# Kernel optimization log

Hardware: AMD Instinct MI355X
Metric: run time of the kernel (lower is better)

Reference implementation:

```python
import jax, jax.numpy as jnp
import numpy as np
from jax import lax

EPS = 1e-9
DN = ('NCHW', 'OIHW', 'NCHW')


def _conv2d_valid(x, w):
    return lax.conv_general_dilated(x, w, window_strides=(1, 1), padding='VALID',
                                    dimension_numbers=DN)


def setup_inputs() -> dict:
    key = jax.random.key(0)
    kx, ky = jax.random.split(key)
    x = jax.random.normal(kx, (32, 64, 96, 96), dtype=jnp.float32)
    y = jax.random.normal(ky, (32, 64, 13, 13), dtype=jnp.float32)  # (K prototypes, C, kh, kw)
    return {'x': x, 'y': y}


def reference(x, y):
    # Per-prototype L2 normalization of y over (C, kh, kw)
    y_norm = jnp.clip(jnp.sqrt(jnp.sum(y * y, axis=(1, 2, 3), keepdims=True)), EPS)
    normed_y = y / y_norm
    # Sliding-window L2 norm of x. The torch code convolves x^2 with ones of
    # shape (K, C, kh, kw) producing K identical channels; we compute one
    # channel and broadcast (same math, less work).
    ones_k = jnp.ones((1,) + y.shape[1:], dtype=x.dtype)
    x_norm = jnp.clip(jnp.sqrt(_conv2d_valid(x * x, ones_k)), EPS)  # (B,1,H',W')
    diss = _conv2d_valid(x, normed_y) / x_norm  # (B,K,H',W')
    return jax.nn.relu(diss)
```

## Files before the change

### kernel.cpp

```cpp
#include <hip/hip_runtime.h>
#include <hip/hip_bf16.h>

#define B_   32
#define C_   64
#define H_   96
#define W_   96
#define K_   32
#define R_   13
#define HO_  84
#define WO_  84
#define HW_  (H_*W_)
#define OHW_ (HO_*WO_)
#define CRR_ (C_*R_*R_)
#define RR_  (R_*R_)

#define TILE_ 16
#define PW_   28
#define NPIX_ (PW_*PW_)
#define RPAD_ 13312
#define BUF_  (2*RPAD_)
#define LDS_NEW (2*BUF_)
#define REGB_ (NPIX_*16)
#define LDS_FB (2*REGB_)

#define XBF_BYTES  ((size_t)B_*4*HW_*32)
#define UG_BYTES   ((size_t)RR_*4096)
#define S_BYTES    ((size_t)B_*HW_*4)
#define INV_BYTES  ((size_t)B_*OHW_*4)
#define WS_NEED    (XBF_BYTES + UG_BYTES + S_BYTES + INV_BYTES)

typedef unsigned int u32;
typedef unsigned short u16;
typedef __attribute__((ext_vector_type(16))) float f32x16;
typedef __attribute__((ext_vector_type(4))) u32 u32x4;

static __device__ __forceinline__ u16 f2bf(float v){
    __hip_bfloat16 h = __float2bfloat16(v);
    return *reinterpret_cast<u16*>(&h);
}

#define MFMA(acc, a, b) asm("v_mfma_f32_32x32x16_bf16 %0, %1, %2, %0" \
                            : "+v"(acc) : "v"(a), "v"(b))

static __device__ __forceinline__ void gload_lds16(const void* g, void* l){
    __builtin_amdgcn_global_load_lds(
        (const __attribute__((address_space(1))) unsigned char*)g,
        (__attribute__((address_space(3))) unsigned char*)l, 16, 0, 0);
}

__global__ void k_prep_y(const float* __restrict__ y, unsigned char* __restrict__ u_g){
    int k = blockIdx.x, tid = threadIdx.x;
    const float* yk = y + (size_t)k * CRR_;
    float ss = 0.f;
    for (int idx = tid; idx < CRR_; idx += 256){ float v = yk[idx]; ss += v*v; }
    for (int off = 32; off; off >>= 1) ss += __shfl_down(ss, off);
    __shared__ float red[4];
    if ((tid & 63) == 0) red[tid >> 6] = ss;
    __syncthreads();
    float inv = 1.f / fmaxf(sqrtf(red[0]+red[1]+red[2]+red[3]), 1e-9f);

    int c = tid & 63, grp = tid >> 6;
    int inoff = (k << 5) | ((c & 15) << 1);
    for (int base = 0; base < RR_; base += 4){
        int ij = base + grp;
        if (ij < RR_){
            int i = ij / R_, jx = ij % R_;
            float v = yk[c*RR_ + ij] * inv;
            size_t slice = ((size_t)(c >> 4) * RR_ + jx*R_ + i) << 10;
            *(u16*)(u_g + slice + inoff) = f2bf(v);
        }
    }
}

__global__ void k_sqcvt(const float* __restrict__ x, float* __restrict__ s,
                        unsigned char* __restrict__ xbf){
    int idx = blockIdx.x*256 + threadIdx.x;
    int b = idx / HW_, r = idx % HW_;
    const float* xb = x + (size_t)b * C_ * HW_ + r;
    float acc = 0.f;
    #pragma unroll
    for (int q = 0; q < 4; ++q){
        int c0 = q*16;
        float a0 = xb[(size_t)(c0+0)*HW_],  a1 = xb[(size_t)(c0+1)*HW_];
        float a2 = xb[(size_t)(c0+2)*HW_],  a3 = xb[(size_t)(c0+3)*HW_];
        float a4 = xb[(size_t)(c0+4)*HW_],  a5 = xb[(size_t)(c0+5)*HW_];
        float a6 = xb[(size_t)(c0+6)*HW_],  a7 = xb[(size_t)(c0+7)*HW_];
        float a8 = xb[(size_t)(c0+8)*HW_],  a9 = xb[(size_t)(c0+9)*HW_];
        float aa = xb[(size_t)(c0+10)*HW_], ab = xb[(size_t)(c0+11)*HW_];
        float ac = xb[(size_t)(c0+12)*HW_], ad = xb[(size_t)(c0+13)*HW_];
        float ae = xb[(size_t)(c0+14)*HW_], af = xb[(size_t)(c0+15)*HW_];
        acc += a0*a0+a1*a1+a2*a2+a3*a3+a4*a4+a5*a5+a6*a6+a7*a7
             + a8*a8+a9*a9+aa*aa+ab*ab+ac*ac+ad*ad+ae*ae+af*af;
        u32x4 q0 = { f2bf(a0)|((u32)f2bf(a1)<<16), f2bf(a2)|((u32)f2bf(a3)<<16),
                     f2bf(a4)|((u32)f2bf(a5)<<16), f2bf(a6)|((u32)f2bf(a7)<<16) };
        u32x4 q1 = { f2bf(a8)|((u32)f2bf(a9)<<16), f2bf(aa)|((u32)f2bf(ab)<<16),
                     f2bf(ac)|((u32)f2bf(ad)<<16), f2bf(ae)|((u32)f2bf(af)<<16) };
        unsigned char* ob = xbf + ((size_t)(b*4 + q)*HW_ + r)*32;
        *(u32x4*)(ob)      = q0;
        *(u32x4*)(ob + 16) = q1;
    }
    s[idx] = acc;
}

__global__ void k_sq(const float* __restrict__ x, float* __restrict__ s){
    int idx = blockIdx.x*256 + threadIdx.x;
    int b = idx / HW_, r = idx % HW_;
    const float* xb = x + (size_t)b * C_ * HW_;
    float acc = 0.f;
    #pragma unroll
    for (int c = 0; c < C_; ++c){ float v = xb[(size_t)c*HW_ + r]; acc += v*v; }
    s[idx] = acc;
}

__global__ void k_inv(const float* __restrict__ s, float* __restrict__ inv_xn){
    int idx = blockIdx.x*256 + threadIdx.x;
    int b = idx / OHW_, r = idx % OHW_;
    int oh = r / WO_, ow = r % WO_;
    const float* sb = s + (size_t)b*HW_ + oh*W_ + ow;
    float acc = 0.f;
    for (int i = 0; i < R_; ++i){
        #pragma unroll
        for (int j = 0; j < R_; ++j) acc += sb[i*W_ + j];
    }
    inv_xn[idx] = 1.f / fmaxf(sqrtf(acc), 1e-9f);
}

__launch_bounds__(256, 4)
__global__ void k_main(const unsigned char* __restrict__ xbf,
                       const unsigned char* __restrict__ u_g,
                       const float* __restrict__ inv_xn, float* __restrict__ out){
    extern __shared__ unsigned char lds[];

    int bb0 = blockIdx.x;
    int bb  = (bb0 & 7) * 144 + (bb0 >> 3);
    int b  = bb / 36;
    int tt = bb % 36;
    int oy = (tt / 6) * TILE_;
    int ox = (tt % 6) * TILE_;

    int tid  = threadIdx.x;
    int lane = tid & 63;
    int wv   = tid >> 6;
    int ks   = lane >> 5;
    int rb   = (lane >> 4) & 1;
    int cx   = lane & 15;
    int kpr  = lane & 31;

    const unsigned char* xq = xbf + (size_t)b*4*HW_*32;
    int aoff = (kpr << 5) + (ks << 4);
    int pb   = (4*wv + rb) * PW_ + cx;

    int goff[13];
    #pragma unroll
    for (int cb = 0; cb < 13; ++cb){
        int p = cb*64 + lane; if (p > NPIX_-1) p = NPIX_-1;
        int py = p / PW_, px = p % PW_;
        int gy = oy + py; if (gy > H_-1) gy = H_-1;
        int gx = ox + px; if (gx > W_-1) gx = W_-1;
        goff[cb] = (gy*W_ + gx) << 5;
    }

#define STAGE(bufsel, q) {                                                   \
        const unsigned char* src = xq + (size_t)(q)*HW_*32;                  \
        unsigned char* dst = lds + (bufsel)*BUF_;                            \
        for (int t = wv; t < 26; t += 4){                                    \
            int h = t & 1, cb = t >> 1;                                      \
            gload_lds16(src + goff[cb] + h*16, dst + h*RPAD_ + cb*1024);     \
        }                                                                    \
    }

    f32x16 acc0 = {}, acc1 = {};
    STAGE(0, 0);

    for (int pass = 0; pass < 4; ++pass){
        __syncthreads();
        if (pass < 3) STAGE((pass+1)&1, pass+1);

        const unsigned char* xh = lds + (pass&1)*BUF_ + ks*RPAD_;
        const unsigned char* ug = u_g + ((size_t)pass*RR_ << 10);

        u32x4 A0 = *(const u32x4*)(ug              + aoff);
        u32x4 A1 = *(const u32x4*)(ug + (1 << 10)  + aoff);
        u32x4 A2 = *(const u32x4*)(ug + (2 << 10)  + aoff);
        u32x4 A3 = *(const u32x4*)(ug + (3 << 10)  + aoff);

        const unsigned char* col0 = xh + pb*16;
        u32x4 d0 = *(const u32x4*)(col0);
        u32x4 d1 = *(const u32x4*)(col0 +   PW_*16);
        u32x4 d2 = *(const u32x4*)(col0 + 2*PW_*16);
        u32x4 d3 = *(const u32x4*)(col0 + 3*PW_*16);
        u32x4 d4 = *(const u32x4*)(col0 + 4*PW_*16);

        int t = 0;
        for (int jx = 0; jx < R_; ++jx){
            const unsigned char* col  = xh + (pb + jx)*16;
            const unsigned char* ncol = col + 16;
            u32x4 e0, e1, e2, e3, e4;
            bool more = (jx < R_-1);
            #pragma unroll
            for (int i = 0; i < R_; ++i, ++t){
                int tn = t + 4; if (tn > RR_-1) tn = RR_-1;
                u32x4 An = *(const u32x4*)(ug + ((size_t)tn << 10) + aoff);
                u32x4 dn = d4;
                if (i < 10) dn = *(const u32x4*)(col + (i+5)*PW_*16);
                if (more){
                    if (i == 8)  e0 = *(const u32x4*)(ncol);
                    if (i == 9)  e1 = *(const u32x4*)(ncol +   PW_*16);
                    if (i == 10) e2 = *(const u32x4*)(ncol + 2*PW_*16);
                    if (i == 11) e3 = *(const u32x4*)(ncol + 3*PW_*16);
                    if (i == 12) e4 = *(const u32x4*)(ncol + 4*PW_*16);
                }
                __builtin_amdgcn_s_setprio(1);
                MFMA(acc0, A0, d0);
                MFMA(acc1, A0, d2);
                __builtin_amdgcn_s_setprio(0);
                A0 = A1; A1 = A2; A2 = A3; A3 = An;
                d0 = d1; d1 = d2; d2 = d3; d3 = d4; d4 = dn;
            }
            if (more){ d0 = e0; d1 = e1; d2 = e2; d3 = e3; d4 = e4; }
        }
    }

    int ow = ox + cx;
#define EPI(ACC, F) {                                                        \
        int oh = oy + 4*wv + rb + 2*(F);                                     \
        bool valid = (oh < HO_) && (ow < WO_);                               \
        float inv = 0.f;                                                     \
        if (valid) inv = inv_xn[(size_t)b*OHW_ + oh*WO_ + ow];               \
        float* ob = out + (size_t)b*K_*OHW_ + oh*WO_ + ow;                   \
        _Pragma("unroll")                                                    \
        for (int r = 0; r < 16; ++r){                                        \
            int kp = (r & 3) + 8*(r >> 2) + 4*ks;                            \
            if (valid) ob[(size_t)kp*OHW_] = fmaxf(ACC[r], 0.f) * inv;       \
        }                                                                    \
    }
    EPI(acc0, 0); EPI(acc1, 1);
#undef EPI
}

__launch_bounds__(256, 4)
__global__ void k_main_fb(const float* __restrict__ x, const unsigned char* __restrict__ u_g,
                          const float* __restrict__ inv_xn, float* __restrict__ out){
    extern __shared__ unsigned char lds[];
    int bb = blockIdx.x;
    int b  = bb / 36;
    int tt = bb % 36;
    int oy = (tt / 6) * TILE_;
    int ox = (tt % 6) * TILE_;
    int tid  = threadIdx.x;
    int lane = tid & 63;
    int wv   = tid >> 6;
    int ks   = lane >> 5;
    int rb   = (lane >> 4) & 1;
    int cx   = lane & 15;
    int kpr  = lane & 31;
    const float* xb = x + (size_t)b * C_ * HW_;
    int aoff = (kpr << 5) + (ks << 4);
    int pb   = (4*wv + rb) * PW_ + cx;
    f32x16 acc0 = {}, acc1 = {};
    for (int pass = 0; pass < 4; ++pass){
        if (pass) __syncthreads();
        int cbase = pass << 4;
        for (int p = tid; p < NPIX_; p += 256){
            int py = p / PW_, px = p % PW_;
            int gy = oy + py; if (gy > H_-1) gy = H_-1;
            int gx = ox + px; if (gx > W_-1) gx = W_-1;
            const float* src = xb + (size_t)cbase*HW_ + gy*W_ + gx;
            u32 w0 = f2bf(src[0*HW_])  | ((u32)f2bf(src[1*HW_])  << 16);
            u32 w1 = f2bf(src[2*HW_])  | ((u32)f2bf(src[3*HW_])  << 16);
            u32 w2 = f2bf(src[4*HW_])  | ((u32)f2bf(src[5*HW_])  << 16);
            u32 w3 = f2bf(src[6*HW_])  | ((u32)f2bf(src[7*HW_])  << 16);
            u32x4 q0 = {w0, w1, w2, w3};
            u32 v0 = f2bf(src[8*HW_])  | ((u32)f2bf(src[9*HW_])  << 16);
            u32 v1 = f2bf(src[10*HW_]) | ((u32)f2bf(src[11*HW_]) << 16);
            u32 v2 = f2bf(src[12*HW_]) | ((u32)f2bf(src[13*HW_]) << 16);
            u32 v3 = f2bf(src[14*HW_]) | ((u32)f2bf(src[15*HW_]) << 16);
            u32x4 q1 = {v0, v1, v2, v3};
            *(u32x4*)(lds +         p*16) = q0;
            *(u32x4*)(lds + REGB_ + p*16) = q1;
        }
        __syncthreads();
        const unsigned char* xh = lds + ks*REGB_;
        const unsigned char* ug = u_g + ((size_t)pass*RR_ << 10);
        u32x4 A0 = *(const u32x4*)(ug              + aoff);
        u32x4 A1 = *(const u32x4*)(ug + (1 << 10)  + aoff);
        u32x4 A2 = *(const u32x4*)(ug + (2 << 10)  + aoff);
        u32x4 A3 = *(const u32x4*)(ug + (3 << 10)  + aoff);
        int t = 0;
        for (int jx = 0; jx < R_; ++jx){
            const unsigned char* col = xh + (pb + jx)*16;
            u32x4 d0 = *(const u32x4*)(col);
            u32x4 d1 = *(const u32x4*)(col +   PW_*16);
            u32x4 d2 = *(const u32x4*)(col + 2*PW_*16);
            u32x4 d3 = *(const u32x4*)(col + 3*PW_*16);
            u32x4 d4 = *(const u32x4*)(col + 4*PW_*16);
            #pragma unroll
            for (int i = 0; i < R_; ++i, ++t){
                int tn = t + 4; if (tn > RR_-1) tn = RR_-1;
                u32x4 An = *(const u32x4*)(ug + ((size_t)tn << 10) + aoff);
                u32x4 dn = d4;
                if (i < 10) dn = *(const u32x4*)(col + (i+5)*PW_*16);
                MFMA(acc0, A0, d0);
                MFMA(acc1, A0, d2);
                A0 = A1; A1 = A2; A2 = A3; A3 = An;
                d0 = d1; d1 = d2; d2 = d3; d3 = d4; d4 = dn;
            }
        }
    }
    int ow = ox + cx;
#define EPI(ACC, F) {                                                        \
        int oh = oy + 4*wv + rb + 2*(F);                                     \
        bool valid = (oh < HO_) && (ow < WO_);                               \
        float inv = 0.f;                                                     \
        if (valid) inv = inv_xn[(size_t)b*OHW_ + oh*WO_ + ow];               \
        float* ob = out + (size_t)b*K_*OHW_ + oh*WO_ + ow;                   \
        _Pragma("unroll")                                                    \
        for (int r = 0; r < 16; ++r){                                        \
            int kp = (r & 3) + 8*(r >> 2) + 4*ks;                            \
            if (valid) ob[(size_t)kp*OHW_] = fmaxf(ACC[r], 0.f) * inv;       \
        }                                                                    \
    }
    EPI(acc0, 0); EPI(acc1, 1);
#undef EPI
}

extern "C" void kernel_launch(void* const* d_in, const int* in_sizes, int n_in,
                              void* d_out, int out_size, void* d_ws, size_t ws_size,
                              hipStream_t stream) {
    const float* x = (const float*)d_in[0];
    const float* y = (const float*)d_in[1];
    float* out = (float*)d_out;
    unsigned char* ws = (unsigned char*)d_ws;

    if (ws_size >= WS_NEED){
        unsigned char* xbf   = ws;
        unsigned char* u_g   = ws + XBF_BYTES;
        float*         s     = (float*)(ws + XBF_BYTES + UG_BYTES);
        float*         invxn = (float*)(ws + XBF_BYTES + UG_BYTES + S_BYTES);

        k_prep_y<<<K_, 256, 0, stream>>>(y, u_g);
        k_sqcvt<<<(B_*HW_)/256, 256, 0, stream>>>(x, s, xbf);
        k_inv<<<(B_*OHW_)/256, 256, 0, stream>>>(s, invxn);
        k_main<<<B_*36, 256, LDS_NEW, stream>>>(xbf, u_g, invxn, out);
    } else {
        unsigned char* u_g   = ws;
        float*         s     = (float*)(ws + UG_BYTES);
        float*         invxn = (float*)(ws + UG_BYTES + S_BYTES);

        k_prep_y<<<K_, 256, 0, stream>>>(y, u_g);
        k_sq<<<(B_*HW_)/256, 256, 0, stream>>>(x, s);
        k_inv<<<(B_*OHW_)/256, 256, 0, stream>>>(s, invxn);
        k_main_fb<<<B_*36, 256, LDS_FB, stream>>>(x, u_g, invxn, out);
    }
}
```

Before: 230.6 us.

## Merge y-prep into x-prep kernel and shrink main-kernel LDS staging buffers

Folds the prototype normalization blocks into the x squaring/bf16 conversion kernel so one launch replaces two. Staging chunks are clamped so the last 64-pixel chunk overlaps the previous one instead of padding, which shrinks each half-buffer from 13312 to 12544 bytes and reduces LDS per block. Launch bounds for the main kernel drop from 4 to 3 blocks per SIMD, which loosens the register limit but may lower occupancy. The overlapping last chunk rewrites a few LDS entries with identical data.

```diff
diff --git a/kernel.cpp b/kernel.cpp
--- a/kernel.cpp
+++ b/kernel.cpp
@@ -17,8 +17,8 @@
 #define TILE_ 16
 #define PW_   28
 #define NPIX_ (PW_*PW_)
-#define RPAD_ 13312
-#define BUF_  (2*RPAD_)
+#define HBUF_ 12544
+#define BUF_  (2*HBUF_)
 #define LDS_NEW (2*BUF_)
 #define REGB_ (NPIX_*16)
 #define LDS_FB (2*REGB_)
@@ -48,13 +48,13 @@
         (__attribute__((address_space(3))) unsigned char*)l, 16, 0, 0);
 }
 
-__global__ void k_prep_y(const float* __restrict__ y, unsigned char* __restrict__ u_g){
-    int k = blockIdx.x, tid = threadIdx.x;
+static __device__ void prep_y_block(const float* __restrict__ y,
+                                    unsigned char* __restrict__ u_g,
+                                    int k, int tid, float* red){
     const float* yk = y + (size_t)k * CRR_;
     float ss = 0.f;
     for (int idx = tid; idx < CRR_; idx += 256){ float v = yk[idx]; ss += v*v; }
     for (int off = 32; off; off >>= 1) ss += __shfl_down(ss, off);
-    __shared__ float red[4];
     if ((tid & 63) == 0) red[tid >> 6] = ss;
     __syncthreads();
     float inv = 1.f / fmaxf(sqrtf(red[0]+red[1]+red[2]+red[3]), 1e-9f);
@@ -72,9 +72,18 @@
     }
 }
 
-__global__ void k_sqcvt(const float* __restrict__ x, float* __restrict__ s,
-                        unsigned char* __restrict__ xbf){
-    int idx = blockIdx.x*256 + threadIdx.x;
+__global__ void k_prep_y(const float* __restrict__ y, unsigned char* __restrict__ u_g){
+    __shared__ float red[4];
+    prep_y_block(y, u_g, blockIdx.x, threadIdx.x, red);
+}
+
+__global__ void k_prep(const float* __restrict__ x, const float* __restrict__ y,
+                       float* __restrict__ s, unsigned char* __restrict__ xbf,
+                       unsigned char* __restrict__ u_g){
+    __shared__ float red[4];
+    int bb = blockIdx.x;
+    if (bb < K_){ prep_y_block(y, u_g, bb, threadIdx.x, red); return; }
+    int idx = (bb - K_)*256 + threadIdx.x;
     int b = idx / HW_, r = idx % HW_;
     const float* xb = x + (size_t)b * C_ * HW_ + r;
     float acc = 0.f;
@@ -125,7 +134,7 @@
     inv_xn[idx] = 1.f / fmaxf(sqrtf(acc), 1e-9f);
 }
 
-__launch_bounds__(256, 4)
+__launch_bounds__(256, 3)
 __global__ void k_main(const unsigned char* __restrict__ xbf,
                        const unsigned char* __restrict__ u_g,
                        const float* __restrict__ inv_xn, float* __restrict__ out){
@@ -150,14 +159,16 @@
     int aoff = (kpr << 5) + (ks << 4);
     int pb   = (4*wv + rb) * PW_ + cx;
 
-    int goff[13];
+    int goff[13], loff[13];
     #pragma unroll
     for (int cb = 0; cb < 13; ++cb){
-        int p = cb*64 + lane; if (p > NPIX_-1) p = NPIX_-1;
+        int cs = cb*64; if (cs > NPIX_-64) cs = NPIX_-64;
+        int p = cs + lane;
         int py = p / PW_, px = p % PW_;
         int gy = oy + py; if (gy > H_-1) gy = H_-1;
         int gx = ox + px; if (gx > W_-1) gx = W_-1;
         goff[cb] = (gy*W_ + gx) << 5;
+        loff[cb] = cs << 4;
     }
 
 #define STAGE(bufsel, q) {                                                   \
@@ -165,7 +176,7 @@
         unsigned char* dst = lds + (bufsel)*BUF_;                            \
         for (int t = wv; t < 26; t += 4){                                    \
             int h = t & 1, cb = t >> 1;                                      \
-            gload_lds16(src + goff[cb] + h*16, dst + h*RPAD_ + cb*1024);     \
+            gload_lds16(src + goff[cb] + h*16, dst + h*HBUF_ + loff[cb]);    \
         }                                                                    \
     }
 
@@ -176,7 +187,7 @@
         __syncthreads();
         if (pass < 3) STAGE((pass+1)&1, pass+1);
 
-        const unsigned char* xh = lds + (pass&1)*BUF_ + ks*RPAD_;
+        const unsigned char* xh = lds + (pass&1)*BUF_ + ks*HBUF_;
         const unsigned char* ug = u_g + ((size_t)pass*RR_ << 10);
 
         u32x4 A0 = *(const u32x4*)(ug              + aoff);
@@ -338,8 +349,7 @@
         float*         s     = (float*)(ws + XBF_BYTES + UG_BYTES);
         float*         invxn = (float*)(ws + XBF_BYTES + UG_BYTES + S_BYTES);
 
-        k_prep_y<<<K_, 256, 0, stream>>>(y, u_g);
-        k_sqcvt<<<(B_*HW_)/256, 256, 0, stream>>>(x, s, xbf);
+        k_prep<<<K_ + (B_*HW_)/256, 256, 0, stream>>>(x, y, s, xbf, u_g);
         k_inv<<<(B_*OHW_)/256, 256, 0, stream>>>(s, invxn);
         k_main<<<B_*36, 256, LDS_NEW, stream>>>(xbf, u_g, invxn, out);
     } else {
```

Result: faster. 225.6 us (-2.2%).
